# Kernel optimization log

Measured on AMD Instinct MI355X. Metric: run time of the kernel, lower is better.

The kernel has to match this reference:

```python
import jax, jax.numpy as jnp
import numpy as np
from jax import lax

B = 16384
ENC_LEN = 48
ENC_HID = 128   # 2 * enc_dim (bidirectional)
DEC_DIM = 32
IN_DIM = 4
T_DEC = 12


def setup_inputs() -> dict:
    key = jax.random.key(0)
    ks = jax.random.split(key, 12)
    f32 = jnp.float32
    return {
        "y": jax.random.normal(ks[0], (B, 13, IN_DIM), f32),
        "encoder_outputs": jax.random.normal(ks[1], (ENC_LEN, B, ENC_HID), f32),
        "hidden": jax.random.normal(ks[2], (B, DEC_DIM), f32),
        "batch_ids": jax.random.randint(ks[3], (B,), 0, 1000),
        "attn_W": jax.random.normal(ks[4], (ENC_LEN, IN_DIM + DEC_DIM), f32) * 0.1,
        "attn_b": jnp.zeros((ENC_LEN,), f32),
        "comb_W": jax.random.normal(ks[5], (IN_DIM, IN_DIM + ENC_HID), f32) * 0.1,
        "comb_b": jnp.zeros((IN_DIM,), f32),
        "w_ih": jax.random.normal(ks[6], (3 * DEC_DIM, IN_DIM), f32) * 0.1,
        "w_hh": jax.random.normal(ks[7], (3 * DEC_DIM, DEC_DIM), f32) * 0.1,
        "b_ih": jnp.zeros((3 * DEC_DIM,), f32),
        "b_hh": jnp.zeros((3 * DEC_DIM,), f32),
        "fc_W": jax.random.normal(ks[8], (1, DEC_DIM), f32) * 0.1,
        "fc_b": jnp.zeros((1,), f32),
    }


def _gru_cell(x, h, w_ih, w_hh, b_ih, b_hh):
    # torch GRU gate ordering: r, z, n
    gi = x @ w_ih.T + b_ih          # (B, 3*DEC_DIM)
    gh = h @ w_hh.T + b_hh
    i_r, i_z, i_n = jnp.split(gi, 3, axis=1)
    h_r, h_z, h_n = jnp.split(gh, 3, axis=1)
    r = jax.nn.sigmoid(i_r + h_r)
    z = jax.nn.sigmoid(i_z + h_z)
    n = jnp.tanh(i_n + r * h_n)
    return (1.0 - z) * n + z * h


def reference(y, encoder_outputs, hidden, batch_ids, attn_W, attn_b,
              comb_W, comb_b, w_ih, w_hh, b_ih, b_hh, fc_W, fc_b):
    # y: (B, 13, 4) -> y_: (13, B, 4); encoder_outputs: (ENC_LEN, B, 128) -> (B, ENC_LEN, 128)
    y_ = jnp.transpose(y, (1, 0, 2))
    enc = jnp.transpose(encoder_outputs, (1, 0, 2))
    x0 = jnp.nan_to_num(y_[0])  # rnn_input[rnn_input != rnn_input] = 0
    # dropout(p=0.5) treated as identity (eval mode)

    def step(carry, y_next3):
        x, h = carry  # x: (B, IN_DIM), h: (B, DEC_DIM)
        # Bahdanau-ish attention: softmax over enc_len positions
        attn_logits = jnp.concatenate([x, h], axis=1) @ attn_W.T + attn_b  # (B, ENC_LEN)
        aw = jax.nn.softmax(attn_logits, axis=1)
        ctx = jnp.einsum('be,bed->bd', aw, enc)  # (B, ENC_HID)
        x2 = jnp.concatenate([ctx, x], axis=1) @ comb_W.T + comb_b  # (B, IN_DIM)
        h = _gru_cell(x2, h, w_ih, w_hh, b_ih, b_hh)
        out = h @ fc_W.T + fc_b  # (B, 1)
        x_next = jnp.concatenate([y_next3, out], axis=1)  # (B, IN_DIM)
        return (x_next, h), out

    xs = y_[1:13, :, 1:]  # (12, B, 3): next-step exogenous features
    (_, _), outs = lax.scan(step, (x0, hidden), xs)  # outs: (12, B, 1)
    y_pred = outs[:, :, 0]  # cat(dim=1).transpose(0,1) -> (12, B)
    return y_pred
```

## Files before the change

kernel.cpp:

```cpp
#include <hip/hip_runtime.h>

#define B 16384
#define ENC_LEN 48
#define ENC_HID 128
#define T_DEC 12

__device__ __forceinline__ float fast_rcp(float x) { return __builtin_amdgcn_rcpf(x); }
__device__ __forceinline__ float fast_exp(float x) { return __expf(x); }
__device__ __forceinline__ float sigmoidf_(float x) { return fast_rcp(1.f + fast_exp(-x)); }
__device__ __forceinline__ float tanhf_(float x) {
    return 1.f - 2.f * fast_rcp(1.f + fast_exp(2.f * x));
}
__device__ __forceinline__ float nan_to_num_(float v) { return (v != v) ? 0.f : v; }

__global__ __launch_bounds__(256) void precompute_P_kernel(
    const float* __restrict__ enc,
    const float* __restrict__ cW,
    float4* __restrict__ P)
{
    const int l = threadIdx.x & 7;
    const int rowLocal = threadIdx.x >> 3;

    float w[4][4][4];
    #pragma unroll
    for (int i = 0; i < 4; ++i)
        #pragma unroll
        for (int k = 0; k < 4; ++k) {
            float4 t = *(const float4*)(cW + i * 132 + k * 32 + l * 4);
            w[i][k][0] = t.x; w[i][k][1] = t.y; w[i][k][2] = t.z; w[i][k][3] = t.w;
        }

    const int totalRows = ENC_LEN * B;
    const int stride = gridDim.x * 32;
    for (int row = blockIdx.x * 32 + rowLocal; row < totalRows; row += stride) {
        const float* r = enc + (size_t)row * ENC_HID;
        float4 e[4];
        #pragma unroll
        for (int k = 0; k < 4; ++k)
            e[k] = *(const float4*)(r + k * 32 + l * 4);

        float a[4];
        #pragma unroll
        for (int i = 0; i < 4; ++i) {
            float s0 = e[0].x * w[i][0][0] + e[0].y * w[i][0][1] + e[0].z * w[i][0][2] + e[0].w * w[i][0][3];
            float s1 = e[1].x * w[i][1][0] + e[1].y * w[i][1][1] + e[1].z * w[i][1][2] + e[1].w * w[i][1][3];
            float s2 = e[2].x * w[i][2][0] + e[2].y * w[i][2][1] + e[2].z * w[i][2][2] + e[2].w * w[i][2][3];
            float s3 = e[3].x * w[i][3][0] + e[3].y * w[i][3][1] + e[3].z * w[i][3][2] + e[3].w * w[i][3][3];
            a[i] = (s0 + s1) + (s2 + s3);
        }
        #pragma unroll
        for (int m = 1; m < 8; m <<= 1) {
            #pragma unroll
            for (int i = 0; i < 4; ++i)
                a[i] += __shfl_xor(a[i], m, 8);
        }
        if (l == 0) P[row] = make_float4(a[0], a[1], a[2], a[3]);
    }
}

__global__ __launch_bounds__(256, 2) void decode_kernel(
    const float* __restrict__ y,
    const float* __restrict__ hidden,
    const float4* __restrict__ P,
    const float* __restrict__ aW,
    const float* __restrict__ ab,
    const float* __restrict__ cW,
    const float* __restrict__ cb,
    const float* __restrict__ wih,
    const float* __restrict__ whh,
    const float* __restrict__ bih,
    const float* __restrict__ bhh,
    const float* __restrict__ fW,
    const float* __restrict__ fb,
    float* __restrict__ out)
{
    __shared__ __align__(16) float aW_l[48 * 36];
    __shared__ __align__(16) float whh_l[96 * 36];
    __shared__ __align__(16) float wih_l[96 * 4];
    __shared__ __align__(16) float hbuf[4][144];

    const int tid = threadIdx.x;

    for (int i = tid; i < 48 * 36; i += 256) aW_l[i] = aW[i];
    for (int i = tid; i < 96 * 32; i += 256) whh_l[(i >> 5) * 36 + (i & 31)] = whh[i];
    for (int i = tid; i < 96 * 4; i += 256) wih_l[i] = wih[i];

    const int lane = tid & 63;
    const int q    = lane & 15;
    const int w    = tid >> 6;
    const int grp  = lane >> 4;
    const int b    = blockIdx.x * 16 + (tid >> 4);

    const float4 pb0 = P[(size_t)(3 * q + 0) * B + b];
    const float4 pb1 = P[(size_t)(3 * q + 1) * B + b];
    const float4 pb2 = P[(size_t)(3 * q + 2) * B + b];

    float h0 = hidden[(size_t)b * 32 + q];
    float h1 = hidden[(size_t)b * 32 + q + 16];

    float xA0 = nan_to_num_(y[(size_t)b * 52 + 0]);
    float xA1 = nan_to_num_(y[(size_t)b * 52 + 1]);
    float xA2 = nan_to_num_(y[(size_t)b * 52 + 2]);
    float xA3 = nan_to_num_(y[(size_t)b * 52 + 3]);

    const float ab0 = ab[3 * q + 0], ab1 = ab[3 * q + 1], ab2 = ab[3 * q + 2];
    const float bi_r0 = bih[q],      bi_z0 = bih[q + 32], bi_n0 = bih[q + 64];
    const float bi_r1 = bih[q + 16], bi_z1 = bih[q + 48], bi_n1 = bih[q + 80];
    const float bh_r0 = bhh[q],      bh_z0 = bhh[q + 32], bh_n0 = bhh[q + 64];
    const float bh_r1 = bhh[q + 16], bh_z1 = bhh[q + 48], bh_n1 = bhh[q + 80];
    const float fw0 = fW[q], fw1 = fW[q + 16];
    const float fb0 = fb[0];
    float cWt[16], cbv[4];
    #pragma unroll
    for (int i = 0; i < 4; ++i) {
        cbv[i] = cb[i];
        #pragma unroll
        for (int k = 0; k < 4; ++k) cWt[i * 4 + k] = cW[i * 132 + 128 + k];
    }

    __syncthreads();

    float* hrow = &hbuf[w][grp * 36];

    int qv = q;

    #pragma unroll 1
    for (int t = 0; t < T_DEC; ++t) {
        asm volatile("" : "+v"(qv));

        const float4* pa0  = (const float4*)(aW_l + (3 * qv + 0) * 36 + 4);
        const float4* pa1  = (const float4*)(aW_l + (3 * qv + 1) * 36 + 4);
        const float4* pa2  = (const float4*)(aW_l + (3 * qv + 2) * 36 + 4);
        const float4* pw0r = (const float4*)(whh_l + (size_t)(qv +  0) * 36);
        const float4* pw0z = (const float4*)(whh_l + (size_t)(qv + 32) * 36);
        const float4* pw0n = (const float4*)(whh_l + (size_t)(qv + 64) * 36);
        const float4* pw1r = (const float4*)(whh_l + (size_t)(qv + 16) * 36);
        const float4* pw1z = (const float4*)(whh_l + (size_t)(qv + 48) * 36);
        const float4* pw1n = (const float4*)(whh_l + (size_t)(qv + 80) * 36);

        float4 yv = make_float4(0.f, 0.f, 0.f, 0.f);
        if (t < T_DEC - 1) yv = *(const float4*)(y + (size_t)b * 52 + (t + 1) * 4);

        hrow[q]      = h0;
        hrow[q + 16] = h1;

        float s0 = 0.f, s1 = 0.f, s2 = 0.f;
        float gr0 = bh_r0, gz0 = bh_z0, gn0 = bh_n0;
        float gr1 = bh_r1, gz1 = bh_z1, gn1 = bh_n1;
        #pragma unroll
        for (int c = 0; c < 8; ++c) {
            const float4 hv = *(const float4*)(hrow + 4 * c);
            float4 wv;
            wv = pa0[c];  s0  += wv.x * hv.x + wv.y * hv.y + wv.z * hv.z + wv.w * hv.w;
            wv = pa1[c];  s1  += wv.x * hv.x + wv.y * hv.y + wv.z * hv.z + wv.w * hv.w;
            wv = pa2[c];  s2  += wv.x * hv.x + wv.y * hv.y + wv.z * hv.z + wv.w * hv.w;
            wv = pw0r[c]; gr0 += wv.x * hv.x + wv.y * hv.y + wv.z * hv.z + wv.w * hv.w;
            wv = pw0z[c]; gz0 += wv.x * hv.x + wv.y * hv.y + wv.z * hv.z + wv.w * hv.w;
            wv = pw0n[c]; gn0 += wv.x * hv.x + wv.y * hv.y + wv.z * hv.z + wv.w * hv.w;
            wv = pw1r[c]; gr1 += wv.x * hv.x + wv.y * hv.y + wv.z * hv.z + wv.w * hv.w;
            wv = pw1z[c]; gz1 += wv.x * hv.x + wv.y * hv.y + wv.z * hv.z + wv.w * hv.w;
            wv = pw1n[c]; gn1 += wv.x * hv.x + wv.y * hv.y + wv.z * hv.z + wv.w * hv.w;
        }

        float4 ax;
        ax = *(const float4*)(aW_l + (3 * qv + 0) * 36);
        const float g0 = fast_exp(s0 + ab0 + ax.x * xA0 + ax.y * xA1 + ax.z * xA2 + ax.w * xA3);
        ax = *(const float4*)(aW_l + (3 * qv + 1) * 36);
        const float g1 = fast_exp(s1 + ab1 + ax.x * xA0 + ax.y * xA1 + ax.z * xA2 + ax.w * xA3);
        ax = *(const float4*)(aW_l + (3 * qv + 2) * 36);
        const float g2 = fast_exp(s2 + ab2 + ax.x * xA0 + ax.y * xA1 + ax.z * xA2 + ax.w * xA3);

        float Sp = g0 + g1 + g2;
        float c0 = g0 * pb0.x + g1 * pb1.x + g2 * pb2.x;
        float c1 = g0 * pb0.y + g1 * pb1.y + g2 * pb2.y;
        float c2 = g0 * pb0.z + g1 * pb1.z + g2 * pb2.z;
        float c3 = g0 * pb0.w + g1 * pb1.w + g2 * pb2.w;

        #pragma unroll
        for (int m = 1; m < 16; m <<= 1) {
            Sp += __shfl_xor(Sp, m);
            c0 += __shfl_xor(c0, m);
            c1 += __shfl_xor(c1, m);
            c2 += __shfl_xor(c2, m);
            c3 += __shfl_xor(c3, m);
        }
        const float rs = fast_rcp(Sp);

        const float x20 = c0 * rs + cWt[ 0] * xA0 + cWt[ 1] * xA1 + cWt[ 2] * xA2 + cWt[ 3] * xA3 + cbv[0];
        const float x21 = c1 * rs + cWt[ 4] * xA0 + cWt[ 5] * xA1 + cWt[ 6] * xA2 + cWt[ 7] * xA3 + cbv[1];
        const float x22 = c2 * rs + cWt[ 8] * xA0 + cWt[ 9] * xA1 + cWt[10] * xA2 + cWt[11] * xA3 + cbv[2];
        const float x23 = c3 * rs + cWt[12] * xA0 + cWt[13] * xA1 + cWt[14] * xA2 + cWt[15] * xA3 + cbv[3];

        float4 wi;
        wi = *(const float4*)(wih_l + (size_t)(qv +  0) * 4);
        const float ir0 = bi_r0 + wi.x * x20 + wi.y * x21 + wi.z * x22 + wi.w * x23;
        wi = *(const float4*)(wih_l + (size_t)(qv + 32) * 4);
        const float iz0 = bi_z0 + wi.x * x20 + wi.y * x21 + wi.z * x22 + wi.w * x23;
        wi = *(const float4*)(wih_l + (size_t)(qv + 64) * 4);
        const float in0 = bi_n0 + wi.x * x20 + wi.y * x21 + wi.z * x22 + wi.w * x23;
        wi = *(const float4*)(wih_l + (size_t)(qv + 16) * 4);
        const float ir1 = bi_r1 + wi.x * x20 + wi.y * x21 + wi.z * x22 + wi.w * x23;
        wi = *(const float4*)(wih_l + (size_t)(qv + 48) * 4);
        const float iz1 = bi_z1 + wi.x * x20 + wi.y * x21 + wi.z * x22 + wi.w * x23;
        wi = *(const float4*)(wih_l + (size_t)(qv + 80) * 4);
        const float in1 = bi_n1 + wi.x * x20 + wi.y * x21 + wi.z * x22 + wi.w * x23;

        const float r0 = sigmoidf_(ir0 + gr0);
        const float z0 = sigmoidf_(iz0 + gz0);
        const float n0 = tanhf_(in0 + r0 * gn0);
        const float hn0 = (1.f - z0) * n0 + z0 * h0;

        const float r1 = sigmoidf_(ir1 + gr1);
        const float z1 = sigmoidf_(iz1 + gz1);
        const float n1 = tanhf_(in1 + r1 * gn1);
        const float hn1 = (1.f - z1) * n1 + z1 * h1;

        float op = fw0 * hn0 + fw1 * hn1;
        #pragma unroll
        for (int m = 1; m < 16; m <<= 1) op += __shfl_xor(op, m);
        const float o = op + fb0;
        if (q == 0) out[(size_t)t * B + b] = o;

        h0 = hn0; h1 = hn1;
        if (t < T_DEC - 1) { xA0 = yv.y; xA1 = yv.z; xA2 = yv.w; xA3 = o; }
    }
}

extern "C" void kernel_launch(void* const* d_in, const int* in_sizes, int n_in,
                              void* d_out, int out_size, void* d_ws, size_t ws_size,
                              hipStream_t stream)
{
    const float* y   = (const float*)d_in[0];
    const float* enc = (const float*)d_in[1];
    const float* hid = (const float*)d_in[2];
    const float* aW  = (const float*)d_in[4];
    const float* ab  = (const float*)d_in[5];
    const float* cW  = (const float*)d_in[6];
    const float* cb  = (const float*)d_in[7];
    const float* wih = (const float*)d_in[8];
    const float* whh = (const float*)d_in[9];
    const float* bih = (const float*)d_in[10];
    const float* bhh = (const float*)d_in[11];
    const float* fW  = (const float*)d_in[12];
    const float* fb  = (const float*)d_in[13];
    float* out = (float*)d_out;

    float4* P = (float4*)d_ws;

    precompute_P_kernel<<<4096, 256, 0, stream>>>(enc, cW, P);
    decode_kernel<<<B / 16, 256, 0, stream>>>(
        y, hid, P, aW, ab, cW, cb, wih, whh, bih, bhh, fW, fb, out);
}
```

Before: 617.6 us.

## Process two batch rows per 16-lane group to reuse shared-memory weight loads

Each 16-lane group in the decode kernel now handles two batch elements instead of one, so every float4 weight read from LDS (attention and hidden-to-hidden weights) feeds two dot products. The input-to-hidden weights and the x-part of the attention weights move from shared memory into registers. The grid is halved to match. In exchange, register pressure roughly doubles for the per-row state, which may reduce occupancy under the 256,2 launch bounds, and there are half as many blocks to spread across the GPU.

```diff
diff --git a/kernel.cpp b/kernel.cpp
--- a/kernel.cpp
+++ b/kernel.cpp
@@ -12,6 +12,9 @@
     return 1.f - 2.f * fast_rcp(1.f + fast_exp(2.f * x));
 }
 __device__ __forceinline__ float nan_to_num_(float v) { return (v != v) ? 0.f : v; }
+__device__ __forceinline__ float dot4(float4 a, float4 b) {
+    return a.x * b.x + a.y * b.y + a.z * b.z + a.w * b.w;
+}
 
 __global__ __launch_bounds__(256) void precompute_P_kernel(
     const float* __restrict__ enc,
@@ -76,32 +79,52 @@
 {
     __shared__ __align__(16) float aW_l[48 * 36];
     __shared__ __align__(16) float whh_l[96 * 36];
-    __shared__ __align__(16) float wih_l[96 * 4];
-    __shared__ __align__(16) float hbuf[4][144];
+    __shared__ __align__(16) float hbuf[4][4][2][36];
 
     const int tid = threadIdx.x;
 
     for (int i = tid; i < 48 * 36; i += 256) aW_l[i] = aW[i];
     for (int i = tid; i < 96 * 32; i += 256) whh_l[(i >> 5) * 36 + (i & 31)] = whh[i];
-    for (int i = tid; i < 96 * 4; i += 256) wih_l[i] = wih[i];
 
     const int lane = tid & 63;
     const int q    = lane & 15;
     const int w    = tid >> 6;
     const int grp  = lane >> 4;
-    const int b    = blockIdx.x * 16 + (tid >> 4);
-
-    const float4 pb0 = P[(size_t)(3 * q + 0) * B + b];
-    const float4 pb1 = P[(size_t)(3 * q + 1) * B + b];
-    const float4 pb2 = P[(size_t)(3 * q + 2) * B + b];
-
-    float h0 = hidden[(size_t)b * 32 + q];
-    float h1 = hidden[(size_t)b * 32 + q + 16];
-
-    float xA0 = nan_to_num_(y[(size_t)b * 52 + 0]);
-    float xA1 = nan_to_num_(y[(size_t)b * 52 + 1]);
-    float xA2 = nan_to_num_(y[(size_t)b * 52 + 2]);
-    float xA3 = nan_to_num_(y[(size_t)b * 52 + 3]);
+    const int gi   = tid >> 4;
+    const int b0   = blockIdx.x * 32 + 2 * gi;
+    const int b1   = b0 + 1;
+
+    const float4 pb0a = P[(size_t)(3 * q + 0) * B + b0];
+    const float4 pb1a = P[(size_t)(3 * q + 1) * B + b0];
+    const float4 pb2a = P[(size_t)(3 * q + 2) * B + b0];
+    const float4 pb0b = P[(size_t)(3 * q + 0) * B + b1];
+    const float4 pb1b = P[(size_t)(3 * q + 1) * B + b1];
+    const float4 pb2b = P[(size_t)(3 * q + 2) * B + b1];
+
+    float h0a = hidden[(size_t)b0 * 32 + q];
+    float h1a = hidden[(size_t)b0 * 32 + q + 16];
+    float h0b = hidden[(size_t)b1 * 32 + q];
+    float h1b = hidden[(size_t)b1 * 32 + q + 16];
+
+    float xa0 = nan_to_num_(y[(size_t)b0 * 52 + 0]);
+    float xa1 = nan_to_num_(y[(size_t)b0 * 52 + 1]);
+    float xa2 = nan_to_num_(y[(size_t)b0 * 52 + 2]);
+    float xa3 = nan_to_num_(y[(size_t)b0 * 52 + 3]);
+    float xb0 = nan_to_num_(y[(size_t)b1 * 52 + 0]);
+    float xb1 = nan_to_num_(y[(size_t)b1 * 52 + 1]);
+    float xb2 = nan_to_num_(y[(size_t)b1 * 52 + 2]);
+    float xb3 = nan_to_num_(y[(size_t)b1 * 52 + 3]);
+
+    const float4 ax0 = *(const float4*)(aW + (3 * q + 0) * 36);
+    const float4 ax1 = *(const float4*)(aW + (3 * q + 1) * 36);
+    const float4 ax2 = *(const float4*)(aW + (3 * q + 2) * 36);
+
+    const float4 wiR0 = *(const float4*)(wih + (size_t)(q +  0) * 4);
+    const float4 wiZ0 = *(const float4*)(wih + (size_t)(q + 32) * 4);
+    const float4 wiN0 = *(const float4*)(wih + (size_t)(q + 64) * 4);
+    const float4 wiR1 = *(const float4*)(wih + (size_t)(q + 16) * 4);
+    const float4 wiZ1 = *(const float4*)(wih + (size_t)(q + 48) * 4);
+    const float4 wiN1 = *(const float4*)(wih + (size_t)(q + 80) * 4);
 
     const float ab0 = ab[3 * q + 0], ab1 = ab[3 * q + 1], ab2 = ab[3 * q + 2];
     const float bi_r0 = bih[q],      bi_z0 = bih[q + 32], bi_n0 = bih[q + 64];
@@ -120,7 +143,8 @@
 
     __syncthreads();
 
-    float* hrow = &hbuf[w][grp * 36];
+    float* hra = &hbuf[w][grp][0][0];
+    float* hrb = &hbuf[w][grp][1][0];
 
     int qv = q;
 
@@ -138,91 +162,124 @@
         const float4* pw1z = (const float4*)(whh_l + (size_t)(qv + 48) * 36);
         const float4* pw1n = (const float4*)(whh_l + (size_t)(qv + 80) * 36);
 
-        float4 yv = make_float4(0.f, 0.f, 0.f, 0.f);
-        if (t < T_DEC - 1) yv = *(const float4*)(y + (size_t)b * 52 + (t + 1) * 4);
-
-        hrow[q]      = h0;
-        hrow[q + 16] = h1;
-
-        float s0 = 0.f, s1 = 0.f, s2 = 0.f;
-        float gr0 = bh_r0, gz0 = bh_z0, gn0 = bh_n0;
-        float gr1 = bh_r1, gz1 = bh_z1, gn1 = bh_n1;
+        float4 yva = make_float4(0.f, 0.f, 0.f, 0.f);
+        float4 yvb = make_float4(0.f, 0.f, 0.f, 0.f);
+        if (t < T_DEC - 1) {
+            yva = *(const float4*)(y + (size_t)b0 * 52 + (t + 1) * 4);
+            yvb = *(const float4*)(y + (size_t)b1 * 52 + (t + 1) * 4);
+        }
+
+        hra[q] = h0a; hra[q + 16] = h1a;
+        hrb[q] = h0b; hrb[q + 16] = h1b;
+
+        float s0a = 0.f, s1a = 0.f, s2a = 0.f;
+        float s0b = 0.f, s1b = 0.f, s2b = 0.f;
+        float gr0a = bh_r0, gz0a = bh_z0, gn0a = bh_n0;
+        float gr1a = bh_r1, gz1a = bh_z1, gn1a = bh_n1;
+        float gr0b = bh_r0, gz0b = bh_z0, gn0b = bh_n0;
+        float gr1b = bh_r1, gz1b = bh_z1, gn1b = bh_n1;
         #pragma unroll
         for (int c = 0; c < 8; ++c) {
-            const float4 hv = *(const float4*)(hrow + 4 * c);
+            const float4 hvA = *(const float4*)(hra + 4 * c);
+            const float4 hvB = *(const float4*)(hrb + 4 * c);
             float4 wv;
-            wv = pa0[c];  s0  += wv.x * hv.x + wv.y * hv.y + wv.z * hv.z + wv.w * hv.w;
-            wv = pa1[c];  s1  += wv.x * hv.x + wv.y * hv.y + wv.z * hv.z + wv.w * hv.w;
-            wv = pa2[c];  s2  += wv.x * hv.x + wv.y * hv.y + wv.z * hv.z + wv.w * hv.w;
-            wv = pw0r[c]; gr0 += wv.x * hv.x + wv.y * hv.y + wv.z * hv.z + wv.w * hv.w;
-            wv = pw0z[c]; gz0 += wv.x * hv.x + wv.y * hv.y + wv.z * hv.z + wv.w * hv.w;
-            wv = pw0n[c]; gn0 += wv.x * hv.x + wv.y * hv.y + wv.z * hv.z + wv.w * hv.w;
-            wv = pw1r[c]; gr1 += wv.x * hv.x + wv.y * hv.y + wv.z * hv.z + wv.w * hv.w;
-            wv = pw1z[c]; gz1 += wv.x * hv.x + wv.y * hv.y + wv.z * hv.z + wv.w * hv.w;
-            wv = pw1n[c]; gn1 += wv.x * hv.x + wv.y * hv.y + wv.z * hv.z + wv.w * hv.w;
-        }
-
-        float4 ax;
-        ax = *(const float4*)(aW_l + (3 * qv + 0) * 36);
-        const float g0 = fast_exp(s0 + ab0 + ax.x * xA0 + ax.y * xA1 + ax.z * xA2 + ax.w * xA3);
-        ax = *(const float4*)(aW_l + (3 * qv + 1) * 36);
-        const float g1 = fast_exp(s1 + ab1 + ax.x * xA0 + ax.y * xA1 + ax.z * xA2 + ax.w * xA3);
-        ax = *(const float4*)(aW_l + (3 * qv + 2) * 36);
-        const float g2 = fast_exp(s2 + ab2 + ax.x * xA0 + ax.y * xA1 + ax.z * xA2 + ax.w * xA3);
-
-        float Sp = g0 + g1 + g2;
-        float c0 = g0 * pb0.x + g1 * pb1.x + g2 * pb2.x;
-        float c1 = g0 * pb0.y + g1 * pb1.y + g2 * pb2.y;
-        float c2 = g0 * pb0.z + g1 * pb1.z + g2 * pb2.z;
-        float c3 = g0 * pb0.w + g1 * pb1.w + g2 * pb2.w;
+            wv = pa0[c];  s0a  += dot4(wv, hvA); s0b  += dot4(wv, hvB);
+            wv = pa1[c];  s1a  += dot4(wv, hvA); s1b  += dot4(wv, hvB);
+            wv = pa2[c];  s2a  += dot4(wv, hvA); s2b  += dot4(wv, hvB);
+            wv = pw0r[c]; gr0a += dot4(wv, hvA); gr0b += dot4(wv, hvB);
+            wv = pw0z[c]; gz0a += dot4(wv, hvA); gz0b += dot4(wv, hvB);
+            wv = pw0n[c]; gn0a += dot4(wv, hvA); gn0b += dot4(wv, hvB);
+            wv = pw1r[c]; gr1a += dot4(wv, hvA); gr1b += dot4(wv, hvB);
+            wv = pw1z[c]; gz1a += dot4(wv, hvA); gz1b += dot4(wv, hvB);
+            wv = pw1n[c]; gn1a += dot4(wv, hvA); gn1b += dot4(wv, hvB);
+        }
+
+        const float g0a = fast_exp(s0a + ab0 + ax0.x * xa0 + ax0.y * xa1 + ax0.z * xa2 + ax0.w * xa3);
+        const float g1a = fast_exp(s1a + ab1 + ax1.x * xa0 + ax1.y * xa1 + ax1.z * xa2 + ax1.w * xa3);
+        const float g2a = fast_exp(s2a + ab2 + ax2.x * xa0 + ax2.y * xa1 + ax2.z * xa2 + ax2.w * xa3);
+        const float g0b = fast_exp(s0b + ab0 + ax0.x * xb0 + ax0.y * xb1 + ax0.z * xb2 + ax0.w * xb3);
+        const float g1b = fast_exp(s1b + ab1 + ax1.x * xb0 + ax1.y * xb1 + ax1.z * xb2 + ax1.w * xb3);
+        const float g2b = fast_exp(s2b + ab2 + ax2.x * xb0 + ax2.y * xb1 + ax2.z * xb2 + ax2.w * xb3);
+
+        float SpA = g0a + g1a + g2a;
+        float c0A = g0a * pb0a.x + g1a * pb1a.x + g2a * pb2a.x;
+        float c1A = g0a * pb0a.y + g1a * pb1a.y + g2a * pb2a.y;
+        float c2A = g0a * pb0a.z + g1a * pb1a.z + g2a * pb2a.z;
+        float c3A = g0a * pb0a.w + g1a * pb1a.w + g2a * pb2a.w;
+        float SpB = g0b + g1b + g2b;
+        float c0B = g0b * pb0b.x + g1b * pb1b.x + g2b * pb2b.x;
+        float c1B = g0b * pb0b.y + g1b * pb1b.y + g2b * pb2b.y;
+        float c2B = g0b * pb0b.z + g1b * pb1b.z + g2b * pb2b.z;
+        float c3B = g0b * pb0b.w + g1b * pb1b.w + g2b * pb2b.w;
 
         #pragma unroll
         for (int m = 1; m < 16; m <<= 1) {
-            Sp += __shfl_xor(Sp, m);
-            c0 += __shfl_xor(c0, m);
-            c1 += __shfl_xor(c1, m);
-            c2 += __shfl_xor(c2, m);
-            c3 += __shfl_xor(c3, m);
-        }
-        const float rs = fast_rcp(Sp);
-
-        const float x20 = c0 * rs + cWt[ 0] * xA0 + cWt[ 1] * xA1 + cWt[ 2] * xA2 + cWt[ 3] * xA3 + cbv[0];
-        const float x21 = c1 * rs + cWt[ 4] * xA0 + cWt[ 5] * xA1 + cWt[ 6] * xA2 + cWt[ 7] * xA3 + cbv[1];
-        const float x22 = c2 * rs + cWt[ 8] * xA0 + cWt[ 9] * xA1 + cWt[10] * xA2 + cWt[11] * xA3 + cbv[2];
-        const float x23 = c3 * rs + cWt[12] * xA0 + cWt[13] * xA1 + cWt[14] * xA2 + cWt[15] * xA3 + cbv[3];
-
-        float4 wi;
-        wi = *(const float4*)(wih_l + (size_t)(qv +  0) * 4);
-        const float ir0 = bi_r0 + wi.x * x20 + wi.y * x21 + wi.z * x22 + wi.w * x23;
-        wi = *(const float4*)(wih_l + (size_t)(qv + 32) * 4);
-        const float iz0 = bi_z0 + wi.x * x20 + wi.y * x21 + wi.z * x22 + wi.w * x23;
-        wi = *(const float4*)(wih_l + (size_t)(qv + 64) * 4);
-        const float in0 = bi_n0 + wi.x * x20 + wi.y * x21 + wi.z * x22 + wi.w * x23;
-        wi = *(const float4*)(wih_l + (size_t)(qv + 16) * 4);
-        const float ir1 = bi_r1 + wi.x * x20 + wi.y * x21 + wi.z * x22 + wi.w * x23;
-        wi = *(const float4*)(wih_l + (size_t)(qv + 48) * 4);
-        const float iz1 = bi_z1 + wi.x * x20 + wi.y * x21 + wi.z * x22 + wi.w * x23;
-        wi = *(const float4*)(wih_l + (size_t)(qv + 80) * 4);
-        const float in1 = bi_n1 + wi.x * x20 + wi.y * x21 + wi.z * x22 + wi.w * x23;
-
-        const float r0 = sigmoidf_(ir0 + gr0);
-        const float z0 = sigmoidf_(iz0 + gz0);
-        const float n0 = tanhf_(in0 + r0 * gn0);
-        const float hn0 = (1.f - z0) * n0 + z0 * h0;
-
-        const float r1 = sigmoidf_(ir1 + gr1);
-        const float z1 = sigmoidf_(iz1 + gz1);
-        const float n1 = tanhf_(in1 + r1 * gn1);
-        const float hn1 = (1.f - z1) * n1 + z1 * h1;
-
-        float op = fw0 * hn0 + fw1 * hn1;
-        #pragma unroll
-        for (int m = 1; m < 16; m <<= 1) op += __shfl_xor(op, m);
-        const float o = op + fb0;
-        if (q == 0) out[(size_t)t * B + b] = o;
-
-        h0 = hn0; h1 = hn1;
-        if (t < T_DEC - 1) { xA0 = yv.y; xA1 = yv.z; xA2 = yv.w; xA3 = o; }
+            SpA += __shfl_xor(SpA, m); SpB += __shfl_xor(SpB, m);
+            c0A += __shfl_xor(c0A, m); c0B += __shfl_xor(c0B, m);
+            c1A += __shfl_xor(c1A, m); c1B += __shfl_xor(c1B, m);
+            c2A += __shfl_xor(c2A, m); c2B += __shfl_xor(c2B, m);
+            c3A += __shfl_xor(c3A, m); c3B += __shfl_xor(c3B, m);
+        }
+        const float rsA = fast_rcp(SpA);
+        const float rsB = fast_rcp(SpB);
+
+        const float x20a = c0A * rsA + cWt[ 0] * xa0 + cWt[ 1] * xa1 + cWt[ 2] * xa2 + cWt[ 3] * xa3 + cbv[0];
+        const float x21a = c1A * rsA + cWt[ 4] * xa0 + cWt[ 5] * xa1 + cWt[ 6] * xa2 + cWt[ 7] * xa3 + cbv[1];
+        const float x22a = c2A * rsA + cWt[ 8] * xa0 + cWt[ 9] * xa1 + cWt[10] * xa2 + cWt[11] * xa3 + cbv[2];
+        const float x23a = c3A * rsA + cWt[12] * xa0 + cWt[13] * xa1 + cWt[14] * xa2 + cWt[15] * xa3 + cbv[3];
+        const float x20b = c0B * rsB + cWt[ 0] * xb0 + cWt[ 1] * xb1 + cWt[ 2] * xb2 + cWt[ 3] * xb3 + cbv[0];
+        const float x21b = c1B * rsB + cWt[ 4] * xb0 + cWt[ 5] * xb1 + cWt[ 6] * xb2 + cWt[ 7] * xb3 + cbv[1];
+        const float x22b = c2B * rsB + cWt[ 8] * xb0 + cWt[ 9] * xb1 + cWt[10] * xb2 + cWt[11] * xb3 + cbv[2];
+        const float x23b = c3B * rsB + cWt[12] * xb0 + cWt[13] * xb1 + cWt[14] * xb2 + cWt[15] * xb3 + cbv[3];
+
+        const float ir0a = bi_r0 + wiR0.x * x20a + wiR0.y * x21a + wiR0.z * x22a + wiR0.w * x23a;
+        const float iz0a = bi_z0 + wiZ0.x * x20a + wiZ0.y * x21a + wiZ0.z * x22a + wiZ0.w * x23a;
+        const float in0a = bi_n0 + wiN0.x * x20a + wiN0.y * x21a + wiN0.z * x22a + wiN0.w * x23a;
+        const float ir1a = bi_r1 + wiR1.x * x20a + wiR1.y * x21a + wiR1.z * x22a + wiR1.w * x23a;
+        const float iz1a = bi_z1 + wiZ1.x * x20a + wiZ1.y * x21a + wiZ1.z * x22a + wiZ1.w * x23a;
+        const float in1a = bi_n1 + wiN1.x * x20a + wiN1.y * x21a + wiN1.z * x22a + wiN1.w * x23a;
+        const float ir0b = bi_r0 + wiR0.x * x20b + wiR0.y * x21b + wiR0.z * x22b + wiR0.w * x23b;
+        const float iz0b = bi_z0 + wiZ0.x * x20b + wiZ0.y * x21b + wiZ0.z * x22b + wiZ0.w * x23b;
+        const float in0b = bi_n0 + wiN0.x * x20b + wiN0.y * x21b + wiN0.z * x22b + wiN0.w * x23b;
+        const float ir1b = bi_r1 + wiR1.x * x20b + wiR1.y * x21b + wiR1.z * x22b + wiR1.w * x23b;
+        const float iz1b = bi_z1 + wiZ1.x * x20b + wiZ1.y * x21b + wiZ1.z * x22b + wiZ1.w * x23b;
+        const float in1b = bi_n1 + wiN1.x * x20b + wiN1.y * x21b + wiN1.z * x22b + wiN1.w * x23b;
+
+        const float r0a = sigmoidf_(ir0a + gr0a);
+        const float z0a = sigmoidf_(iz0a + gz0a);
+        const float n0a = tanhf_(in0a + r0a * gn0a);
+        const float hn0a = (1.f - z0a) * n0a + z0a * h0a;
+        const float r1a = sigmoidf_(ir1a + gr1a);
+        const float z1a = sigmoidf_(iz1a + gz1a);
+        const float n1a = tanhf_(in1a + r1a * gn1a);
+        const float hn1a = (1.f - z1a) * n1a + z1a * h1a;
+
+        const float r0b = sigmoidf_(ir0b + gr0b);
+        const float z0b = sigmoidf_(iz0b + gz0b);
+        const float n0b = tanhf_(in0b + r0b * gn0b);
+        const float hn0b = (1.f - z0b) * n0b + z0b * h0b;
+        const float r1b = sigmoidf_(ir1b + gr1b);
+        const float z1b = sigmoidf_(iz1b + gz1b);
+        const float n1b = tanhf_(in1b + r1b * gn1b);
+        const float hn1b = (1.f - z1b) * n1b + z1b * h1b;
+
+        float opA = fw0 * hn0a + fw1 * hn1a;
+        float opB = fw0 * hn0b + fw1 * hn1b;
+        #pragma unroll
+        for (int m = 1; m < 16; m <<= 1) {
+            opA += __shfl_xor(opA, m);
+            opB += __shfl_xor(opB, m);
+        }
+        const float oA = opA + fb0;
+        const float oB = opB + fb0;
+        if (q == 0) out[(size_t)t * B + b0] = oA;
+        if (q == 1) out[(size_t)t * B + b1] = oB;
+
+        h0a = hn0a; h1a = hn1a; h0b = hn0b; h1b = hn1b;
+        if (t < T_DEC - 1) {
+            xa0 = yva.y; xa1 = yva.z; xa2 = yva.w; xa3 = oA;
+            xb0 = yvb.y; xb1 = yvb.z; xb2 = yvb.w; xb3 = oB;
+        }
     }
 }
 
@@ -248,6 +305,6 @@
     float4* P = (float4*)d_ws;
 
     precompute_P_kernel<<<4096, 256, 0, stream>>>(enc, cW, P);
-    decode_kernel<<<B / 16, 256, 0, stream>>>(
+    decode_kernel<<<B / 32, 256, 0, stream>>>(
         y, hid, P, aW, ab, cW, cb, wih, whh, bih, bhh, fW, fb, out);
 }
```

New measurement: 632.8 us. 1.02x slower.

## Fuse encoder projection into decode kernel via per-block shared-memory P

Applied to the files above, without the earlier changes.

Removes the separate precompute kernel. Each decode block now projects its own 16 batch rows of encoder outputs through comb_W into a shared-memory P tile, so the global P round trip and one launch go away. Attention x-weights and w_ih rows are hoisted into registers, and launch bounds are raised to allow four blocks per CU. In exchange, each block does a 48x16-row encoder streaming pass before decoding, which may load-balance worse than the grid-stride precompute. Register pressure is higher while the occupancy target is tighter, so spills are possible.

```diff
diff --git a/kernel.cpp b/kernel.cpp
--- a/kernel.cpp
+++ b/kernel.cpp
@@ -13,55 +13,10 @@
 }
 __device__ __forceinline__ float nan_to_num_(float v) { return (v != v) ? 0.f : v; }
 
-__global__ __launch_bounds__(256) void precompute_P_kernel(
-    const float* __restrict__ enc,
-    const float* __restrict__ cW,
-    float4* __restrict__ P)
-{
-    const int l = threadIdx.x & 7;
-    const int rowLocal = threadIdx.x >> 3;
-
-    float w[4][4][4];
-    #pragma unroll
-    for (int i = 0; i < 4; ++i)
-        #pragma unroll
-        for (int k = 0; k < 4; ++k) {
-            float4 t = *(const float4*)(cW + i * 132 + k * 32 + l * 4);
-            w[i][k][0] = t.x; w[i][k][1] = t.y; w[i][k][2] = t.z; w[i][k][3] = t.w;
-        }
-
-    const int totalRows = ENC_LEN * B;
-    const int stride = gridDim.x * 32;
-    for (int row = blockIdx.x * 32 + rowLocal; row < totalRows; row += stride) {
-        const float* r = enc + (size_t)row * ENC_HID;
-        float4 e[4];
-        #pragma unroll
-        for (int k = 0; k < 4; ++k)
-            e[k] = *(const float4*)(r + k * 32 + l * 4);
-
-        float a[4];
-        #pragma unroll
-        for (int i = 0; i < 4; ++i) {
-            float s0 = e[0].x * w[i][0][0] + e[0].y * w[i][0][1] + e[0].z * w[i][0][2] + e[0].w * w[i][0][3];
-            float s1 = e[1].x * w[i][1][0] + e[1].y * w[i][1][1] + e[1].z * w[i][1][2] + e[1].w * w[i][1][3];
-            float s2 = e[2].x * w[i][2][0] + e[2].y * w[i][2][1] + e[2].z * w[i][2][2] + e[2].w * w[i][2][3];
-            float s3 = e[3].x * w[i][3][0] + e[3].y * w[i][3][1] + e[3].z * w[i][3][2] + e[3].w * w[i][3][3];
-            a[i] = (s0 + s1) + (s2 + s3);
-        }
-        #pragma unroll
-        for (int m = 1; m < 8; m <<= 1) {
-            #pragma unroll
-            for (int i = 0; i < 4; ++i)
-                a[i] += __shfl_xor(a[i], m, 8);
-        }
-        if (l == 0) P[row] = make_float4(a[0], a[1], a[2], a[3]);
-    }
-}
-
-__global__ __launch_bounds__(256, 2) void decode_kernel(
+__global__ __launch_bounds__(256, 4) void fused_kernel(
     const float* __restrict__ y,
     const float* __restrict__ hidden,
-    const float4* __restrict__ P,
+    const float* __restrict__ enc,
     const float* __restrict__ aW,
     const float* __restrict__ ab,
     const float* __restrict__ cW,
@@ -76,24 +31,64 @@
 {
     __shared__ __align__(16) float aW_l[48 * 36];
     __shared__ __align__(16) float whh_l[96 * 36];
-    __shared__ __align__(16) float wih_l[96 * 4];
     __shared__ __align__(16) float hbuf[4][144];
+    __shared__ __align__(16) float4 P_l[ENC_LEN * 16];
 
     const int tid = threadIdx.x;
 
     for (int i = tid; i < 48 * 36; i += 256) aW_l[i] = aW[i];
     for (int i = tid; i < 96 * 32; i += 256) whh_l[(i >> 5) * 36 + (i & 31)] = whh[i];
-    for (int i = tid; i < 96 * 4; i += 256) wih_l[i] = wih[i];
+
+    {
+        const int l = tid & 7;
+        const int rowLocal = tid >> 3;
+        const int bBase = blockIdx.x * 16;
+
+        float w[4][4][4];
+        #pragma unroll
+        for (int i = 0; i < 4; ++i)
+            #pragma unroll
+            for (int k = 0; k < 4; ++k) {
+                float4 t = *(const float4*)(cW + i * 132 + k * 32 + l * 4);
+                w[i][k][0] = t.x; w[i][k][1] = t.y; w[i][k][2] = t.z; w[i][k][3] = t.w;
+            }
+
+        #pragma unroll 2
+        for (int p = 0; p < 24; ++p) {
+            const int rho = p * 32 + rowLocal;
+            const int e   = rho >> 4;
+            const int bL  = rho & 15;
+            const float* r = enc + ((size_t)e * B + bBase + bL) * ENC_HID;
+            float4 e4[4];
+            #pragma unroll
+            for (int k = 0; k < 4; ++k)
+                e4[k] = *(const float4*)(r + k * 32 + l * 4);
+
+            float a[4];
+            #pragma unroll
+            for (int i = 0; i < 4; ++i) {
+                float s0 = e4[0].x * w[i][0][0] + e4[0].y * w[i][0][1] + e4[0].z * w[i][0][2] + e4[0].w * w[i][0][3];
+                float s1 = e4[1].x * w[i][1][0] + e4[1].y * w[i][1][1] + e4[1].z * w[i][1][2] + e4[1].w * w[i][1][3];
+                float s2 = e4[2].x * w[i][2][0] + e4[2].y * w[i][2][1] + e4[2].z * w[i][2][2] + e4[2].w * w[i][2][3];
+                float s3 = e4[3].x * w[i][3][0] + e4[3].y * w[i][3][1] + e4[3].z * w[i][3][2] + e4[3].w * w[i][3][3];
+                a[i] = (s0 + s1) + (s2 + s3);
+            }
+            #pragma unroll
+            for (int m = 1; m < 8; m <<= 1) {
+                #pragma unroll
+                for (int i = 0; i < 4; ++i)
+                    a[i] += __shfl_xor(a[i], m, 8);
+            }
+            if (l == 0) P_l[rho] = make_float4(a[0], a[1], a[2], a[3]);
+        }
+    }
 
     const int lane = tid & 63;
     const int q    = lane & 15;
     const int w    = tid >> 6;
     const int grp  = lane >> 4;
-    const int b    = blockIdx.x * 16 + (tid >> 4);
-
-    const float4 pb0 = P[(size_t)(3 * q + 0) * B + b];
-    const float4 pb1 = P[(size_t)(3 * q + 1) * B + b];
-    const float4 pb2 = P[(size_t)(3 * q + 2) * B + b];
+    const int gi   = tid >> 4;
+    const int b    = blockIdx.x * 16 + gi;
 
     float h0 = hidden[(size_t)b * 32 + q];
     float h1 = hidden[(size_t)b * 32 + q + 16];
@@ -102,6 +97,17 @@
     float xA1 = nan_to_num_(y[(size_t)b * 52 + 1]);
     float xA2 = nan_to_num_(y[(size_t)b * 52 + 2]);
     float xA3 = nan_to_num_(y[(size_t)b * 52 + 3]);
+
+    const float4 ax0 = *(const float4*)(aW + (3 * q + 0) * 36);
+    const float4 ax1 = *(const float4*)(aW + (3 * q + 1) * 36);
+    const float4 ax2 = *(const float4*)(aW + (3 * q + 2) * 36);
+
+    const float4 wiR0 = *(const float4*)(wih + (size_t)(q +  0) * 4);
+    const float4 wiZ0 = *(const float4*)(wih + (size_t)(q + 32) * 4);
+    const float4 wiN0 = *(const float4*)(wih + (size_t)(q + 64) * 4);
+    const float4 wiR1 = *(const float4*)(wih + (size_t)(q + 16) * 4);
+    const float4 wiZ1 = *(const float4*)(wih + (size_t)(q + 48) * 4);
+    const float4 wiN1 = *(const float4*)(wih + (size_t)(q + 80) * 4);
 
     const float ab0 = ab[3 * q + 0], ab1 = ab[3 * q + 1], ab2 = ab[3 * q + 2];
     const float bi_r0 = bih[q],      bi_z0 = bih[q + 32], bi_n0 = bih[q + 64];
@@ -119,6 +125,10 @@
     }
 
     __syncthreads();
+
+    const float4 pb0 = P_l[(3 * q + 0) * 16 + gi];
+    const float4 pb1 = P_l[(3 * q + 1) * 16 + gi];
+    const float4 pb2 = P_l[(3 * q + 2) * 16 + gi];
 
     float* hrow = &hbuf[w][grp * 36];
 
@@ -162,13 +172,9 @@
             wv = pw1n[c]; gn1 += wv.x * hv.x + wv.y * hv.y + wv.z * hv.z + wv.w * hv.w;
         }
 
-        float4 ax;
-        ax = *(const float4*)(aW_l + (3 * qv + 0) * 36);
-        const float g0 = fast_exp(s0 + ab0 + ax.x * xA0 + ax.y * xA1 + ax.z * xA2 + ax.w * xA3);
-        ax = *(const float4*)(aW_l + (3 * qv + 1) * 36);
-        const float g1 = fast_exp(s1 + ab1 + ax.x * xA0 + ax.y * xA1 + ax.z * xA2 + ax.w * xA3);
-        ax = *(const float4*)(aW_l + (3 * qv + 2) * 36);
-        const float g2 = fast_exp(s2 + ab2 + ax.x * xA0 + ax.y * xA1 + ax.z * xA2 + ax.w * xA3);
+        const float g0 = fast_exp(s0 + ab0 + ax0.x * xA0 + ax0.y * xA1 + ax0.z * xA2 + ax0.w * xA3);
+        const float g1 = fast_exp(s1 + ab1 + ax1.x * xA0 + ax1.y * xA1 + ax1.z * xA2 + ax1.w * xA3);
+        const float g2 = fast_exp(s2 + ab2 + ax2.x * xA0 + ax2.y * xA1 + ax2.z * xA2 + ax2.w * xA3);
 
         float Sp = g0 + g1 + g2;
         float c0 = g0 * pb0.x + g1 * pb1.x + g2 * pb2.x;
@@ -191,19 +197,12 @@
         const float x22 = c2 * rs + cWt[ 8] * xA0 + cWt[ 9] * xA1 + cWt[10] * xA2 + cWt[11] * xA3 + cbv[2];
         const float x23 = c3 * rs + cWt[12] * xA0 + cWt[13] * xA1 + cWt[14] * xA2 + cWt[15] * xA3 + cbv[3];
 
-        float4 wi;
-        wi = *(const float4*)(wih_l + (size_t)(qv +  0) * 4);
-        const float ir0 = bi_r0 + wi.x * x20 + wi.y * x21 + wi.z * x22 + wi.w * x23;
-        wi = *(const float4*)(wih_l + (size_t)(qv + 32) * 4);
-        const float iz0 = bi_z0 + wi.x * x20 + wi.y * x21 + wi.z * x22 + wi.w * x23;
-        wi = *(const float4*)(wih_l + (size_t)(qv + 64) * 4);
-        const float in0 = bi_n0 + wi.x * x20 + wi.y * x21 + wi.z * x22 + wi.w * x23;
-        wi = *(const float4*)(wih_l + (size_t)(qv + 16) * 4);
-        const float ir1 = bi_r1 + wi.x * x20 + wi.y * x21 + wi.z * x22 + wi.w * x23;
-        wi = *(const float4*)(wih_l + (size_t)(qv + 48) * 4);
-        const float iz1 = bi_z1 + wi.x * x20 + wi.y * x21 + wi.z * x22 + wi.w * x23;
-        wi = *(const float4*)(wih_l + (size_t)(qv + 80) * 4);
-        const float in1 = bi_n1 + wi.x * x20 + wi.y * x21 + wi.z * x22 + wi.w * x23;
+        const float ir0 = bi_r0 + wiR0.x * x20 + wiR0.y * x21 + wiR0.z * x22 + wiR0.w * x23;
+        const float iz0 = bi_z0 + wiZ0.x * x20 + wiZ0.y * x21 + wiZ0.z * x22 + wiZ0.w * x23;
+        const float in0 = bi_n0 + wiN0.x * x20 + wiN0.y * x21 + wiN0.z * x22 + wiN0.w * x23;
+        const float ir1 = bi_r1 + wiR1.x * x20 + wiR1.y * x21 + wiR1.z * x22 + wiR1.w * x23;
+        const float iz1 = bi_z1 + wiZ1.x * x20 + wiZ1.y * x21 + wiZ1.z * x22 + wiZ1.w * x23;
+        const float in1 = bi_n1 + wiN1.x * x20 + wiN1.y * x21 + wiN1.z * x22 + wiN1.w * x23;
 
         const float r0 = sigmoidf_(ir0 + gr0);
         const float z0 = sigmoidf_(iz0 + gz0);
@@ -245,9 +244,8 @@
     const float* fb  = (const float*)d_in[13];
     float* out = (float*)d_out;
 
-    float4* P = (float4*)d_ws;
-
-    precompute_P_kernel<<<4096, 256, 0, stream>>>(enc, cW, P);
-    decode_kernel<<<B / 16, 256, 0, stream>>>(
-        y, hid, P, aW, ab, cW, cb, wih, whh, bih, bhh, fW, fb, out);
+    (void)d_ws; (void)ws_size;
+
+    fused_kernel<<<B / 16, 256, 0, stream>>>(
+        y, hid, enc, aW, ab, cW, cb, wih, whh, bih, bhh, fW, fb, out);
 }
```

After: 622.3 us. No clear change (+0.8%).
